# Kernel optimization log

Hardware: AMD Instinct MI355X
Metric: run time of the kernel (lower is better)

Reference implementation:

```python
import jax
import jax.numpy as jnp
import numpy as np

B, N, C_IN, C_OUT, K = 16, 4096, 64, 128, 16
RATIO = 0.25
M = int(RATIO * N)  # 1024 sampled points per cloud
EPS = 1e-5


def setup_inputs() -> dict:
    key = jax.random.key(0)
    ks = jax.random.split(key, 4)
    features = jax.random.normal(ks[0], (B, N, C_IN), dtype=jnp.float32)
    positions = jax.random.normal(ks[1], (B, N, 3), dtype=jnp.float32)
    batch = jnp.repeat(jnp.arange(B, dtype=jnp.int64), N)  # [B*N]
    W = jax.random.normal(ks[2], (C_IN, C_OUT), dtype=jnp.float32) * 0.1
    b = jax.random.normal(ks[3], (C_OUT,), dtype=jnp.float32) * 0.1
    gamma = jnp.ones((C_OUT,), dtype=jnp.float32)
    beta = jnp.zeros((C_OUT,), dtype=jnp.float32)
    return {"features": features, "positions": positions, "batch": batch,
            "W": W, "b": b, "gamma": gamma, "beta": beta}


def _fps_single(pos):
    """Farthest point sampling on one cloud. pos: [N,3] -> indices [M] (start at 0)."""
    def step(carry, _):
        min_d, last = carry
        d = jnp.sum((pos - pos[last]) ** 2, axis=-1)       # [N]
        min_d = jnp.minimum(min_d, d)
        nxt = jnp.argmax(min_d).astype(jnp.int32)
        return (min_d, nxt), nxt
    init = (jnp.full((N,), 1e10, dtype=pos.dtype), jnp.int32(0))
    _, rest = jax.lax.scan(step, init, None, length=M - 1)
    return jnp.concatenate([jnp.zeros((1,), jnp.int32), rest])


def reference(features, positions, batch, W, b, gamma, beta):
    # --- FPS per batch (on positions) ---
    fps_idx = jax.vmap(_fps_single)(positions)                     # [B, M] int32

    # --- MLP: Linear + BatchNorm1d (training-mode batch stats over all B*N points) ---
    h = jnp.einsum('bnc,co->bno', features, W) + b                 # [B, N, C_OUT]
    flat = h.reshape(-1, C_OUT)
    mean = jnp.mean(flat, axis=0)
    var = jnp.mean((flat - mean) ** 2, axis=0)                     # biased, as BN
    hn = (h - mean) * jax.lax.rsqrt(var + EPS) * gamma + beta      # [B, N, C_OUT]

    # --- kNN in FEATURE space: queries = sampled features, keys = all features ---
    q = jnp.take_along_axis(features, fps_idx[..., None], axis=1)  # [B, M, C_IN]
    d2 = (jnp.sum(q * q, -1)[:, :, None]
          + jnp.sum(features * features, -1)[:, None, :]
          - 2.0 * jnp.einsum('bmd,bnd->bmn', q, features))         # [B, M, N]
    _, nbr = jax.lax.top_k(-d2, K)                                 # [B, M, K]

    # --- gather MLP'd features at neighbors, max-pool per sampled point ---
    gathered = jnp.take_along_axis(hn, nbr.reshape(B, M * K)[..., None], axis=1)
    new_features = gathered.reshape(B, M, K, C_OUT).max(axis=2)    # [B, M, C_OUT]

    new_positions = jnp.take_along_axis(positions, fps_idx[..., None], axis=1)  # [B, M, 3]
    new_batch = jnp.take_along_axis(batch.reshape(B, N), fps_idx.astype(jnp.int64), axis=1).reshape(-1)
    return new_features, new_positions, new_batch
```

## Files before the change

kernel.cpp:

```cpp
#include <hip/hip_runtime.h>

#define B_ 16
#define N_ 4096
#define CIN_ 64
#define COUT_ 128
#define K_ 16
#define M_ 1024

typedef float f32x2 __attribute__((ext_vector_type(2)));
typedef unsigned long long u64;

#define DPPF(m, ctrl)                                                          \
  m = fmaxf(m, __int_as_float(__builtin_amdgcn_update_dpp(                     \
                  0, __float_as_int(m), ctrl, 0xF, 0xF, true)))
#define DPPI(e, ctrl)                                                          \
  e = max(e, __builtin_amdgcn_update_dpp(0, e, ctrl, 0xF, 0xF, true))

__device__ __forceinline__ unsigned mono32(float d) {
  unsigned u = __float_as_uint(d);
  return u ^ (unsigned)(((int)u >> 31) | 0x80000000);
}

__device__ __forceinline__ unsigned short f2bf(float x) {
  const unsigned u = __float_as_uint(x);
  return (unsigned short)((u + 0x7FFF + ((u >> 16) & 1)) >> 16);
}
__device__ __forceinline__ float bf2f(unsigned short s) {
  return __uint_as_float((unsigned)s << 16);
}

__global__ __launch_bounds__(512) void mega_kernel(
    const float* __restrict__ pos, const float* __restrict__ features,
    const float* __restrict__ W, const float* __restrict__ bias,
    int* __restrict__ fps_idx, unsigned short* __restrict__ h,
    float* __restrict__ stats, int* __restrict__ prog,
    u64* __restrict__ cand, int S) {
  __shared__ __align__(16) char smem[84 * 1024];
  const int id = blockIdx.x;
  const int t = threadIdx.x;

  if (id < B_) {
    const int b = id;
    float4* P = (float4*)smem;
    volatile u64* red = (volatile u64*)(smem + 65536);
    const float* pb = pos + (size_t)b * N_ * 3;
    if (t < 8) ((u64*)(smem + 65536))[t] = 0;
    for (int i = t; i < N_; i += 512)
      P[i] = make_float4(pb[i * 3], pb[i * 3 + 1], pb[i * 3 + 2], 0.f);
    __syncthreads();
    if (t >= 256) return;
    f32x2 px[8], py[8], pz[8], md[8];
#pragma unroll
    for (int j = 0; j < 8; ++j) {
      const float4 lo = P[t + 512 * j];
      const float4 hi = P[t + 512 * j + 256];
      px[j] = (f32x2){lo.x, hi.x};
      py[j] = (f32x2){lo.y, hi.y};
      pz[j] = (f32x2){lo.z, hi.z};
      md[j] = (f32x2){1e10f, 1e10f};
    }
    if (t == 0) fps_idx[b * M_] = 0;
    const int wv = t >> 6, ln = t & 63;
    const int e0 = 65535 - t;
    float4 lp = P[0];
    for (int step = 1; step < M_; ++step) {
      const f32x2 lx = {lp.x, lp.x}, ly = {lp.y, lp.y}, lz = {lp.z, lp.z};
      float bestd = -1.0f;
      int be = 0;
      {
#pragma clang fp contract(off)
#pragma unroll
        for (int j = 0; j < 8; ++j) {
          const f32x2 dx = px[j] - lx;
          const f32x2 dy = py[j] - ly;
          const f32x2 dz = pz[j] - lz;
          const f32x2 s1 = dx * dx;
          const f32x2 s2 = dy * dy;
          const f32x2 s3 = dz * dz;
          const f32x2 d = (s1 + s2) + s3;
          f32x2 nd;
          nd.x = fminf(md[j].x, d.x);
          nd.y = fminf(md[j].y, d.y);
          md[j] = nd;
          if (nd.x > bestd) { bestd = nd.x; be = e0 - (j << 9); }
          if (nd.y > bestd) { bestd = nd.y; be = e0 - (j << 9) - 256; }
        }
      }
      float m = bestd;
      DPPF(m, 0x111); DPPF(m, 0x112); DPPF(m, 0x114); DPPF(m, 0x118);
      DPPF(m, 0x142); DPPF(m, 0x143);
      const float wm =
          __int_as_float(__builtin_amdgcn_readlane(__float_as_int(m), 63));
      int enc = (bestd == wm) ? be : 0;
      DPPI(enc, 0x111); DPPI(enc, 0x112); DPPI(enc, 0x114); DPPI(enc, 0x118);
      DPPI(enc, 0x142); DPPI(enc, 0x143);
      const int wenc = __builtin_amdgcn_readlane(enc, 63);
      const unsigned tag = (unsigned)(step & 1023);
      volatile u64* rb = red + (step & 1) * 4;
      if (ln == 0)
        rb[wv] = ((u64)__float_as_uint(wm) << 32) | ((u64)tag << 16) |
                 (unsigned)wenc;
      u64 r0, r1, r2, r3;
      for (;;) {
        r0 = rb[0]; r1 = rb[1]; r2 = rb[2]; r3 = rb[3];
        const u64 x = ((r0 >> 16) ^ tag) | ((r1 >> 16) ^ tag) |
                      ((r2 >> 16) ^ tag) | ((r3 >> 16) ^ tag);
        if (!(x & 0x3FF)) break;
      }
      u64 rr = r0 > r1 ? r0 : r1;
      const u64 rc = r2 > r3 ? r2 : r3;
      if (rc > rr) rr = rc;
      const int last = 65535 - (int)(unsigned)(rr & 0xFFFFu);
      lp = P[last];
      if (t == 0) {
        fps_idx[b * M_ + step] = last;
        if ((step & 63) == 63)
          __hip_atomic_store(&prog[b], (step >> 6) + 1, __ATOMIC_RELEASE,
                             __HIP_MEMORY_SCOPE_AGENT);
      }
    }
    return;
  }

  if (id < B_ + 512) {
    const int lid = id - B_;
    float* ls = (float*)smem;
    for (int i = t; i < 256; i += 512) ls[i] = 0.f;
    __syncthreads();
    const int o4 = (t & 31) << 2;
    const int rl = t >> 5;
    const float4 bv = *(const float4*)(bias + o4);
    float4 s4 = {0, 0, 0, 0}, ss4 = {0, 0, 0, 0};
    for (int i = 0; i < 8; ++i) {
      const int r = lid * 128 + rl * 8 + i;
      const float4* fr = (const float4*)(features + (size_t)r * CIN_);
      float4 acc = bv;
#pragma unroll
      for (int c4 = 0; c4 < 16; ++c4) {
        const float4 fv = fr[c4];
        const float* wr = W + (size_t)(c4 * 4) * COUT_ + o4;
        const float4 w0 = *(const float4*)(wr);
        const float4 w1 = *(const float4*)(wr + COUT_);
        const float4 w2 = *(const float4*)(wr + 2 * COUT_);
        const float4 w3 = *(const float4*)(wr + 3 * COUT_);
        acc.x = fmaf(fv.x, w0.x, acc.x); acc.y = fmaf(fv.x, w0.y, acc.y);
        acc.z = fmaf(fv.x, w0.z, acc.z); acc.w = fmaf(fv.x, w0.w, acc.w);
        acc.x = fmaf(fv.y, w1.x, acc.x); acc.y = fmaf(fv.y, w1.y, acc.y);
        acc.z = fmaf(fv.y, w1.z, acc.z); acc.w = fmaf(fv.y, w1.w, acc.w);
        acc.x = fmaf(fv.z, w2.x, acc.x); acc.y = fmaf(fv.z, w2.y, acc.y);
        acc.z = fmaf(fv.z, w2.z, acc.z); acc.w = fmaf(fv.z, w2.w, acc.w);
        acc.x = fmaf(fv.w, w3.x, acc.x); acc.y = fmaf(fv.w, w3.y, acc.y);
        acc.z = fmaf(fv.w, w3.z, acc.z); acc.w = fmaf(fv.w, w3.w, acc.w);
      }
      *(ushort4*)(h + (size_t)r * COUT_ + o4) =
          make_ushort4(f2bf(acc.x), f2bf(acc.y), f2bf(acc.z), f2bf(acc.w));
      s4.x += acc.x; s4.y += acc.y; s4.z += acc.z; s4.w += acc.w;
      ss4.x = fmaf(acc.x, acc.x, ss4.x); ss4.y = fmaf(acc.y, acc.y, ss4.y);
      ss4.z = fmaf(acc.z, acc.z, ss4.z); ss4.w = fmaf(acc.w, acc.w, ss4.w);
    }
    atomicAdd(&ls[o4 + 0], s4.x); atomicAdd(&ls[o4 + 1], s4.y);
    atomicAdd(&ls[o4 + 2], s4.z); atomicAdd(&ls[o4 + 3], s4.w);
    atomicAdd(&ls[128 + o4 + 0], ss4.x); atomicAdd(&ls[128 + o4 + 1], ss4.y);
    atomicAdd(&ls[128 + o4 + 2], ss4.z); atomicAdd(&ls[128 + o4 + 3], ss4.w);
    __syncthreads();
    if (t < 128) {
      atomicAdd(&stats[t], ls[t]);
      atomicAdd(&stats[128 + t], ls[128 + t]);
    }
    return;
  }

  {
    const int kid = id - (B_ + 512);
    const int qt = kid / (B_ * S);
    const int rem = kid % (B_ * S);
    const int b = rem / S;
    const int s = rem % S;
    const int KPS = N_ / S;
    const int KT = KPS / 128;
    float* Qs = (float*)smem;
    float* Ks = (float*)(smem + 16384);
    float* sd2 = (float*)(smem + 49152);
    float* qq = (float*)(smem + 82944);
    float* ff = (float*)(smem + 83200);
    int* qid = (int*)(smem + 83712);
    const float* fb = features + (size_t)b * N_ * CIN_;

    if (t == 0) {
      while (__hip_atomic_load(&prog[b], __ATOMIC_ACQUIRE,
                               __HIP_MEMORY_SCOPE_AGENT) < qt + 1)
        __builtin_amdgcn_s_sleep(16);
    }
    __syncthreads();
    if (t < 64) qid[t] = fps_idx[b * M_ + qt * 64 + t];
    __syncthreads();
#pragma unroll
    for (int st = 0; st < 2; ++st) {
      const int iid = t + 512 * st;
      const int row = iid >> 4, c4 = iid & 15;
      const int pc = (c4 + (row >> 2)) & 15;
      const float4 v = *(const float4*)(fb + (size_t)qid[row] * CIN_ + c4 * 4);
      *(float4*)(&Qs[row * 64 + pc * 4]) = v;
    }
    __syncthreads();
    if (t < 64) {
      float sv = 0.f;
#pragma unroll
      for (int c4 = 0; c4 < 16; ++c4) {
        const int pc = (c4 + (t >> 2)) & 15;
        const float4 v = *(const float4*)(&Qs[t * 64 + pc * 4]);
        sv = fmaf(v.x, v.x, sv); sv = fmaf(v.y, v.y, sv);
        sv = fmaf(v.z, v.z, sv); sv = fmaf(v.w, v.w, sv);
      }
      qq[t] = sv;
    }

    u64 lst[16];
#pragma unroll
    for (int p = 0; p < 16; ++p) lst[p] = ~0ull;
    u64 worst = ~0ull;
    int wpos = 0;

    const int q0 = (t >> 5) * 4;
    const int k0 = (t & 31) * 4;
    const int sq = t >> 3;
    const int ssub = t & 7;

    for (int kt = 0; kt < KT; ++kt) {
      const int kb = s * KPS + kt * 128;
#pragma unroll
      for (int st = 0; st < 4; ++st) {
        const int iid = t + 512 * st;
        const int row = iid >> 4, c4 = iid & 15;
        const int pc = (c4 + (row >> 2)) & 15;
        const float4 v =
            *(const float4*)(fb + (size_t)(kb + row) * CIN_ + c4 * 4);
        *(float4*)(&Ks[row * 64 + pc * 4]) = v;
      }
      __syncthreads();
      if (t < 128) {
        float sv = 0.f;
#pragma unroll
        for (int c4 = 0; c4 < 16; ++c4) {
          const int pc = (c4 + (t >> 2)) & 15;
          const float4 v = *(const float4*)(&Ks[t * 64 + pc * 4]);
          sv = fmaf(v.x, v.x, sv); sv = fmaf(v.y, v.y, sv);
          sv = fmaf(v.z, v.z, sv); sv = fmaf(v.w, v.w, sv);
        }
        ff[t] = sv;
      }
      __syncthreads();
      float acc[4][4];
#pragma unroll
      for (int i = 0; i < 4; ++i)
#pragma unroll
        for (int j = 0; j < 4; ++j) acc[i][j] = 0.f;
#pragma unroll
      for (int c4 = 0; c4 < 16; ++c4) {
        float4 qv[4], kv[4];
#pragma unroll
        for (int i = 0; i < 4; ++i) {
          const int row = q0 + i;
          const int pc = (c4 + (row >> 2)) & 15;
          qv[i] = *(const float4*)(&Qs[row * 64 + pc * 4]);
        }
#pragma unroll
        for (int j = 0; j < 4; ++j) {
          const int row = k0 + j;
          const int pc = (c4 + (row >> 2)) & 15;
          kv[j] = *(const float4*)(&Ks[row * 64 + pc * 4]);
        }
#pragma unroll
        for (int i = 0; i < 4; ++i)
#pragma unroll
          for (int j = 0; j < 4; ++j) {
            acc[i][j] = fmaf(qv[i].x, kv[j].x, acc[i][j]);
            acc[i][j] = fmaf(qv[i].y, kv[j].y, acc[i][j]);
            acc[i][j] = fmaf(qv[i].z, kv[j].z, acc[i][j]);
            acc[i][j] = fmaf(qv[i].w, kv[j].w, acc[i][j]);
          }
      }
#pragma unroll
      for (int i = 0; i < 4; ++i) {
        const float qv = qq[q0 + i];
        float4 o;
        o.x = __fsub_rn(__fadd_rn(qv, ff[k0 + 0]), 2.f * acc[i][0]);
        o.y = __fsub_rn(__fadd_rn(qv, ff[k0 + 1]), 2.f * acc[i][1]);
        o.z = __fsub_rn(__fadd_rn(qv, ff[k0 + 2]), 2.f * acc[i][2]);
        o.w = __fsub_rn(__fadd_rn(qv, ff[k0 + 3]), 2.f * acc[i][3]);
        *(float4*)(&sd2[(q0 + i) * 132 + k0]) = o;
      }
      __syncthreads();
#pragma unroll
      for (int g = 0; g < 4; ++g) {
        const float4 v = *(const float4*)(&sd2[sq * 132 + ssub * 16 + g * 4]);
        const float dv[4] = {v.x, v.y, v.z, v.w};
#pragma unroll
        for (int jj = 0; jj < 4; ++jj) {
          const int key = kb + ssub * 16 + g * 4 + jj;
          const u64 pk = ((u64)mono32(dv[jj]) << 32) | (unsigned)key;
          if (pk < worst) {
#pragma unroll
            for (int p = 0; p < 16; ++p)
              if (p == wpos) lst[p] = pk;
            worst = lst[0]; wpos = 0;
#pragma unroll
            for (int p = 1; p < 16; ++p)
              if (lst[p] > worst) { worst = lst[p]; wpos = p; }
          }
        }
      }
      __syncthreads();
    }
    u64* cb = cand + ((size_t)(b * M_ + qt * 64 + sq) * S + s) * 16;
    for (int r = 0; r < K_; ++r) {
      u64 mn = lst[0];
#pragma unroll
      for (int p = 1; p < 16; ++p)
        if (lst[p] < mn) mn = lst[p];
      u64 m2 = mn;
#pragma unroll
      for (int off = 1; off < 8; off <<= 1) {
        const u64 o = __shfl_xor(m2, off, 64);
        if (o < m2) m2 = o;
      }
      if (mn == m2) {
        bool done = false;
#pragma unroll
        for (int p = 0; p < 16; ++p)
          if (!done && lst[p] == m2) { lst[p] = ~0ull; done = true; }
      }
      if (ssub == 0) cb[r] = m2;
    }
  }
}

__global__ void finalize_kernel(float* __restrict__ stats,
                                const float* __restrict__ gamma,
                                const float* __restrict__ beta) {
  const int o = threadIdx.x;
  const float inv = 1.0f / (float)(B_ * N_);
  const float mean = stats[o] * inv;
  const float var = stats[128 + o] * inv - mean * mean;
  const float r = 1.0f / sqrtf(var + 1e-5f);
  const float sc = gamma[o] * r;
  stats[256 + o] = sc;
  stats[384 + o] = beta[o] - mean * sc;
}

__global__ __launch_bounds__(256) void gather_kernel(
    const unsigned short* __restrict__ h, const float* __restrict__ stats,
    const u64* __restrict__ cand, float* __restrict__ out, int S) {
  const int g = blockIdx.x;
  const int t = threadIdx.x;
  const int S16 = S * 16;
  __shared__ u64 cl[2][128];
  __shared__ int nbi[32];
  const int Q0 = g * 2;
  if (t < 2 * S16) {
    const int qi = t / S16, sl = t % S16;
    cl[qi][sl] = cand[(size_t)(Q0 + qi) * S16 + sl];
  }
  __syncthreads();
  if ((t & 127) == 0) {
    const int qi = t >> 7;
    int ptr[8] = {0, 0, 0, 0, 0, 0, 0, 0};
    for (int r = 0; r < K_; ++r) {
      u64 mn = ~0ull;
      int ms = 0;
      for (int s = 0; s < S; ++s) {
        if (ptr[s] < 16) {
          const u64 v = cl[qi][s * 16 + ptr[s]];
          if (v < mn) { mn = v; ms = s; }
        }
      }
      nbi[qi * 16 + r] = (int)(unsigned)(mn & 0xFFFFFFFFu);
      ptr[ms]++;
    }
  }
  __syncthreads();
  const int q2 = t >> 7, o = t & 127;
  const int Q = Q0 + q2, b = Q >> 10;
  const float sc = stats[256 + o];
  const float sh = stats[384 + o];
  float mx = -3.402823466e38f;
#pragma unroll
  for (int k = 0; k < K_; ++k) {
    const int n = nbi[q2 * 16 + k];
    const float v = fmaf(bf2f(h[((size_t)b * N_ + n) * COUT_ + o]), sc, sh);
    mx = fmaxf(mx, v);
  }
  out[(size_t)Q * COUT_ + o] = mx;
}

__global__ __launch_bounds__(256) void tail_kernel(const float* __restrict__ pos,
                                                   const int* __restrict__ fps_idx,
                                                   float* __restrict__ out,
                                                   int batch_as_i64) {
  const int gid = blockIdx.x * 256 + threadIdx.x;
  const int A = B_ * M_ * COUT_;
  const int P = B_ * M_ * 3;
  if (gid < P) {
    const int Q = gid / 3;
    const int c = gid - Q * 3;
    const int b = Q >> 10;
    const int idx = fps_idx[Q];
    out[A + gid] = pos[((size_t)b * N_ + idx) * 3 + c];
  } else {
    const int Q = gid - P;
    if (Q < B_ * M_) {
      const int b = Q >> 10;
      float* base = out + A + P;
      if (batch_as_i64)
        ((long long*)base)[Q] = (long long)b;
      else
        base[Q] = (float)b;
    }
  }
}

extern "C" void kernel_launch(void* const* d_in, const int* in_sizes, int n_in,
                              void* d_out, int out_size, void* d_ws, size_t ws_size,
                              hipStream_t stream) {
  const float* features = (const float*)d_in[0];
  const float* positions = (const float*)d_in[1];
  const float* W = (const float*)d_in[3];
  const float* bias = (const float*)d_in[4];
  const float* gamma = (const float*)d_in[5];
  const float* beta = (const float*)d_in[6];
  float* out = (float*)d_out;
  unsigned char* ws = (unsigned char*)d_ws;

  int* fps_idx = (int*)ws;
  unsigned short* h = (unsigned short*)(ws + 65536);
  const size_t hoff = 65536 + (size_t)B_ * N_ * COUT_ * 2;
  float* stats = (float*)(ws + hoff);
  int* prog = (int*)(ws + hoff + 2048);
  u64* cand = (u64*)(ws + hoff + 2048 + 256);
  const size_t base = hoff + 2048 + 256;

  int S = 8;
  while (S > 1 && base + (size_t)B_ * M_ * S * 16 * 8 > ws_size) S >>= 1;

  const int rem = out_size - (B_ * M_ * COUT_) - (B_ * M_ * 3);
  const int batch_as_i64 = (rem >= 2 * B_ * M_) ? 1 : 0;

  hipMemsetAsync(stats, 0, 2048 + 256, stream);
  mega_kernel<<<B_ + 512 + 256 * S, 512, 0, stream>>>(
      positions, features, W, bias, fps_idx, h, stats, prog, cand, S);
  finalize_kernel<<<1, 128, 0, stream>>>(stats, gamma, beta);
  gather_kernel<<<B_ * M_ / 2, 256, 0, stream>>>(h, stats, cand, out, S);
  tail_kernel<<<256, 256, 0, stream>>>(positions, fps_idx, out, batch_as_i64);
}
```

Baseline: 1.043 ms.

## Fuse BN finalize, neighbor gather and tail into persistent mega kernel

Moves the BatchNorm finalize step into the last linear block, which it detects with an atomic counter, and signals completion through a flag. The kNN block that finishes last for each query tile now does the candidate merge, the vectorized bf16 gather with max-pool, and the position and batch output writes. This removes three separate kernel launches and their serialization tail. The FPS cross-wave reduction also changes from a spin-poll on tagged LDS slots to __syncthreads, so the idle upper waves now have to loop through matching barriers. This adds inter-block dependencies and the risk of a spin-wait on stats_flag.

New measurement: 1.062 ms. No clear change (+1.8%).

```diff
diff --git a/kernel.cpp b/kernel.cpp
--- a/kernel.cpp
+++ b/kernel.cpp
@@ -20,104 +20,103 @@
   unsigned u = __float_as_uint(d);
   return u ^ (unsigned)(((int)u >> 31) | 0x80000000);
 }
-
 __device__ __forceinline__ unsigned short f2bf(float x) {
   const unsigned u = __float_as_uint(x);
   return (unsigned short)((u + 0x7FFF + ((u >> 16) & 1)) >> 16);
 }
-__device__ __forceinline__ float bf2f(unsigned short s) {
-  return __uint_as_float((unsigned)s << 16);
-}
 
 __global__ __launch_bounds__(512) void mega_kernel(
     const float* __restrict__ pos, const float* __restrict__ features,
     const float* __restrict__ W, const float* __restrict__ bias,
+    const float* __restrict__ gamma, const float* __restrict__ beta,
     int* __restrict__ fps_idx, unsigned short* __restrict__ h,
-    float* __restrict__ stats, int* __restrict__ prog,
-    u64* __restrict__ cand, int S) {
+    float* __restrict__ ctrl, u64* __restrict__ cand,
+    float* __restrict__ out, int S, int batch_as_i64) {
   __shared__ __align__(16) char smem[84 * 1024];
   const int id = blockIdx.x;
   const int t = threadIdx.x;
+  float* stats = ctrl;
+  int* prog = (int*)(ctrl + 512);
+  int* lin_done = (int*)(ctrl + 528);
+  int* stats_flag = (int*)(ctrl + 529);
+  int* qt_done = (int*)(ctrl + 544);
+  const int A = B_ * M_ * COUT_;
+  const int P = B_ * M_ * 3;
 
   if (id < B_) {
     const int b = id;
-    float4* P = (float4*)smem;
-    volatile u64* red = (volatile u64*)(smem + 65536);
+    float4* Pp = (float4*)smem;
+    u64* red = (u64*)(smem + 65536);
     const float* pb = pos + (size_t)b * N_ * 3;
-    if (t < 8) ((u64*)(smem + 65536))[t] = 0;
     for (int i = t; i < N_; i += 512)
-      P[i] = make_float4(pb[i * 3], pb[i * 3 + 1], pb[i * 3 + 2], 0.f);
-    __syncthreads();
-    if (t >= 256) return;
-    f32x2 px[8], py[8], pz[8], md[8];
-#pragma unroll
-    for (int j = 0; j < 8; ++j) {
-      const float4 lo = P[t + 512 * j];
-      const float4 hi = P[t + 512 * j + 256];
-      px[j] = (f32x2){lo.x, hi.x};
-      py[j] = (f32x2){lo.y, hi.y};
-      pz[j] = (f32x2){lo.z, hi.z};
-      md[j] = (f32x2){1e10f, 1e10f};
-    }
-    if (t == 0) fps_idx[b * M_] = 0;
-    const int wv = t >> 6, ln = t & 63;
-    const int e0 = 65535 - t;
-    float4 lp = P[0];
-    for (int step = 1; step < M_; ++step) {
-      const f32x2 lx = {lp.x, lp.x}, ly = {lp.y, lp.y}, lz = {lp.z, lp.z};
-      float bestd = -1.0f;
-      int be = 0;
-      {
+      Pp[i] = make_float4(pb[i * 3], pb[i * 3 + 1], pb[i * 3 + 2], 0.f);
+    __syncthreads();
+    if (t < 256) {
+      f32x2 px[8], py[8], pz[8], md[8];
+#pragma unroll
+      for (int j = 0; j < 8; ++j) {
+        const float4 lo = Pp[t + 512 * j];
+        const float4 hi = Pp[t + 512 * j + 256];
+        px[j] = (f32x2){lo.x, hi.x};
+        py[j] = (f32x2){lo.y, hi.y};
+        pz[j] = (f32x2){lo.z, hi.z};
+        md[j] = (f32x2){1e10f, 1e10f};
+      }
+      if (t == 0) fps_idx[b * M_] = 0;
+      const int wv = t >> 6, ln = t & 63;
+      const int e0 = 65535 - t;
+      float4 lp = Pp[0];
+      for (int step = 1; step < M_; ++step) {
+        const f32x2 lx = {lp.x, lp.x}, ly = {lp.y, lp.y}, lz = {lp.z, lp.z};
+        float bestd = -1.0f;
+        int be = 0;
+        {
 #pragma clang fp contract(off)
 #pragma unroll
-        for (int j = 0; j < 8; ++j) {
-          const f32x2 dx = px[j] - lx;
-          const f32x2 dy = py[j] - ly;
-          const f32x2 dz = pz[j] - lz;
-          const f32x2 s1 = dx * dx;
-          const f32x2 s2 = dy * dy;
-          const f32x2 s3 = dz * dz;
-          const f32x2 d = (s1 + s2) + s3;
-          f32x2 nd;
-          nd.x = fminf(md[j].x, d.x);
-          nd.y = fminf(md[j].y, d.y);
-          md[j] = nd;
-          if (nd.x > bestd) { bestd = nd.x; be = e0 - (j << 9); }
-          if (nd.y > bestd) { bestd = nd.y; be = e0 - (j << 9) - 256; }
-        }
-      }
-      float m = bestd;
-      DPPF(m, 0x111); DPPF(m, 0x112); DPPF(m, 0x114); DPPF(m, 0x118);
-      DPPF(m, 0x142); DPPF(m, 0x143);
-      const float wm =
-          __int_as_float(__builtin_amdgcn_readlane(__float_as_int(m), 63));
-      int enc = (bestd == wm) ? be : 0;
-      DPPI(enc, 0x111); DPPI(enc, 0x112); DPPI(enc, 0x114); DPPI(enc, 0x118);
-      DPPI(enc, 0x142); DPPI(enc, 0x143);
-      const int wenc = __builtin_amdgcn_readlane(enc, 63);
-      const unsigned tag = (unsigned)(step & 1023);
-      volatile u64* rb = red + (step & 1) * 4;
-      if (ln == 0)
-        rb[wv] = ((u64)__float_as_uint(wm) << 32) | ((u64)tag << 16) |
-                 (unsigned)wenc;
-      u64 r0, r1, r2, r3;
-      for (;;) {
-        r0 = rb[0]; r1 = rb[1]; r2 = rb[2]; r3 = rb[3];
-        const u64 x = ((r0 >> 16) ^ tag) | ((r1 >> 16) ^ tag) |
-                      ((r2 >> 16) ^ tag) | ((r3 >> 16) ^ tag);
-        if (!(x & 0x3FF)) break;
-      }
-      u64 rr = r0 > r1 ? r0 : r1;
-      const u64 rc = r2 > r3 ? r2 : r3;
-      if (rc > rr) rr = rc;
-      const int last = 65535 - (int)(unsigned)(rr & 0xFFFFu);
-      lp = P[last];
-      if (t == 0) {
-        fps_idx[b * M_ + step] = last;
-        if ((step & 63) == 63)
-          __hip_atomic_store(&prog[b], (step >> 6) + 1, __ATOMIC_RELEASE,
-                             __HIP_MEMORY_SCOPE_AGENT);
-      }
+          for (int j = 0; j < 8; ++j) {
+            const f32x2 dx = px[j] - lx;
+            const f32x2 dy = py[j] - ly;
+            const f32x2 dz = pz[j] - lz;
+            const f32x2 s1 = dx * dx;
+            const f32x2 s2 = dy * dy;
+            const f32x2 s3 = dz * dz;
+            const f32x2 d = (s1 + s2) + s3;
+            f32x2 nd;
+            nd.x = fminf(md[j].x, d.x);
+            nd.y = fminf(md[j].y, d.y);
+            md[j] = nd;
+            if (nd.x > bestd) { bestd = nd.x; be = e0 - (j << 9); }
+            if (nd.y > bestd) { bestd = nd.y; be = e0 - (j << 9) - 256; }
+          }
+        }
+        float m = bestd;
+        DPPF(m, 0x111); DPPF(m, 0x112); DPPF(m, 0x114); DPPF(m, 0x118);
+        DPPF(m, 0x142); DPPF(m, 0x143);
+        const float wm =
+            __int_as_float(__builtin_amdgcn_readlane(__float_as_int(m), 63));
+        int enc = (bestd == wm) ? be : 0;
+        DPPI(enc, 0x111); DPPI(enc, 0x112); DPPI(enc, 0x114); DPPI(enc, 0x118);
+        DPPI(enc, 0x142); DPPI(enc, 0x143);
+        const int wenc = __builtin_amdgcn_readlane(enc, 63);
+        if (ln == 0)
+          red[(step & 1) * 4 + wv] =
+              ((u64)__float_as_uint(wm) << 32) | (unsigned)wenc;
+        __syncthreads();
+        const u64* rb = &red[(step & 1) * 4];
+        u64 rr = rb[0] > rb[1] ? rb[0] : rb[1];
+        const u64 r2 = rb[2] > rb[3] ? rb[2] : rb[3];
+        if (r2 > rr) rr = r2;
+        const int last = 65535 - (int)(unsigned)(rr & 0xFFFFu);
+        lp = Pp[last];
+        if (t == 0) {
+          fps_idx[b * M_ + step] = last;
+          if ((step & 63) == 63)
+            __hip_atomic_store(&prog[b], (step >> 6) + 1, __ATOMIC_RELEASE,
+                               __HIP_MEMORY_SCOPE_AGENT);
+        }
+      }
+    } else {
+      for (int step = 1; step < M_; ++step) __syncthreads();
     }
     return;
   }
@@ -167,6 +166,26 @@
       atomicAdd(&stats[t], ls[t]);
       atomicAdd(&stats[128 + t], ls[128 + t]);
     }
+    __syncthreads();
+    int* lastf = (int*)(smem + 1024);
+    if (t == 0)
+      *lastf = (__hip_atomic_fetch_add(lin_done, 1, __ATOMIC_ACQ_REL,
+                                       __HIP_MEMORY_SCOPE_AGENT) == 511);
+    __syncthreads();
+    if (!*lastf) return;
+    if (t < 128) {
+      const float inv = 1.0f / (float)(B_ * N_);
+      const float mean = stats[t] * inv;
+      const float var = stats[128 + t] * inv - mean * mean;
+      const float r = 1.0f / sqrtf(var + 1e-5f);
+      const float sc = gamma[t] * r;
+      stats[256 + t] = sc;
+      stats[384 + t] = beta[t] - mean * sc;
+    }
+    __syncthreads();
+    if (t == 0)
+      __hip_atomic_store(stats_flag, 1, __ATOMIC_RELEASE,
+                         __HIP_MEMORY_SCOPE_AGENT);
     return;
   }
 
@@ -184,6 +203,7 @@
     float* qq = (float*)(smem + 82944);
     float* ff = (float*)(smem + 83200);
     int* qid = (int*)(smem + 83712);
+    int* mflag = (int*)(smem + 83968);
     const float* fb = features + (size_t)b * N_ * CIN_;
 
     if (t == 0) {
@@ -332,84 +352,84 @@
       }
       if (ssub == 0) cb[r] = m2;
     }
-  }
-}
-
-__global__ void finalize_kernel(float* __restrict__ stats,
-                                const float* __restrict__ gamma,
-                                const float* __restrict__ beta) {
-  const int o = threadIdx.x;
-  const float inv = 1.0f / (float)(B_ * N_);
-  const float mean = stats[o] * inv;
-  const float var = stats[128 + o] * inv - mean * mean;
-  const float r = 1.0f / sqrtf(var + 1e-5f);
-  const float sc = gamma[o] * r;
-  stats[256 + o] = sc;
-  stats[384 + o] = beta[o] - mean * sc;
-}
-
-__global__ __launch_bounds__(256) void gather_kernel(
-    const unsigned short* __restrict__ h, const float* __restrict__ stats,
-    const u64* __restrict__ cand, float* __restrict__ out, int S) {
-  const int g = blockIdx.x;
-  const int t = threadIdx.x;
-  const int S16 = S * 16;
-  __shared__ u64 cl[2][128];
-  __shared__ int nbi[32];
-  const int Q0 = g * 2;
-  if (t < 2 * S16) {
-    const int qi = t / S16, sl = t % S16;
-    cl[qi][sl] = cand[(size_t)(Q0 + qi) * S16 + sl];
-  }
-  __syncthreads();
-  if ((t & 127) == 0) {
-    const int qi = t >> 7;
-    int ptr[8] = {0, 0, 0, 0, 0, 0, 0, 0};
-    for (int r = 0; r < K_; ++r) {
-      u64 mn = ~0ull;
-      int ms = 0;
-      for (int s = 0; s < S; ++s) {
-        if (ptr[s] < 16) {
-          const u64 v = cl[qi][s * 16 + ptr[s]];
-          if (v < mn) { mn = v; ms = s; }
-        }
-      }
-      nbi[qi * 16 + r] = (int)(unsigned)(mn & 0xFFFFFFFFu);
-      ptr[ms]++;
-    }
-  }
-  __syncthreads();
-  const int q2 = t >> 7, o = t & 127;
-  const int Q = Q0 + q2, b = Q >> 10;
-  const float sc = stats[256 + o];
-  const float sh = stats[384 + o];
-  float mx = -3.402823466e38f;
-#pragma unroll
-  for (int k = 0; k < K_; ++k) {
-    const int n = nbi[q2 * 16 + k];
-    const float v = fmaf(bf2f(h[((size_t)b * N_ + n) * COUT_ + o]), sc, sh);
-    mx = fmaxf(mx, v);
-  }
-  out[(size_t)Q * COUT_ + o] = mx;
-}
-
-__global__ __launch_bounds__(256) void tail_kernel(const float* __restrict__ pos,
-                                                   const int* __restrict__ fps_idx,
-                                                   float* __restrict__ out,
-                                                   int batch_as_i64) {
-  const int gid = blockIdx.x * 256 + threadIdx.x;
-  const int A = B_ * M_ * COUT_;
-  const int P = B_ * M_ * 3;
-  if (gid < P) {
-    const int Q = gid / 3;
-    const int c = gid - Q * 3;
-    const int b = Q >> 10;
-    const int idx = fps_idx[Q];
-    out[A + gid] = pos[((size_t)b * N_ + idx) * 3 + c];
-  } else {
-    const int Q = gid - P;
-    if (Q < B_ * M_) {
-      const int b = Q >> 10;
+    __syncthreads();
+    if (t == 0)
+      *mflag = (__hip_atomic_fetch_add(&qt_done[b * 16 + qt], 1,
+                                       __ATOMIC_ACQ_REL,
+                                       __HIP_MEMORY_SCOPE_AGENT) == S - 1);
+    __syncthreads();
+    if (!*mflag) return;
+
+    u64* cl = (u64*)smem;
+    int* nbi = (int*)(smem + 65536);
+    float* scsh = (float*)(smem + 69632);
+    if (t == 0) {
+      while (__hip_atomic_load(stats_flag, __ATOMIC_ACQUIRE,
+                               __HIP_MEMORY_SCOPE_AGENT) == 0)
+        __builtin_amdgcn_s_sleep(8);
+    }
+    __syncthreads();
+    const int S16 = S * 16;
+    const u64* cg = cand + (size_t)(b * M_ + qt * 64) * S16;
+    for (int i = t; i < 64 * S16; i += 512) cl[i] = cg[i];
+    if (t < 256) scsh[t] = stats[256 + t];
+    __syncthreads();
+    if (t < 64) {
+      int ptr[8] = {0, 0, 0, 0, 0, 0, 0, 0};
+      for (int r = 0; r < K_; ++r) {
+        u64 mn = ~0ull;
+        int ms = 0;
+        for (int ss = 0; ss < S; ++ss) {
+          if (ptr[ss] < 16) {
+            const u64 v = cl[t * S16 + ss * 16 + ptr[ss]];
+            if (v < mn) { mn = v; ms = ss; }
+          }
+        }
+        nbi[t * 16 + r] = (int)(unsigned)(mn & 0xFFFFFFFFu);
+        ptr[ms]++;
+      }
+    }
+    __syncthreads();
+    {
+      const int q = t >> 3;
+      const int c0 = (t & 7) * 16;
+      float sc[16], sh[16], mx[16];
+#pragma unroll
+      for (int i = 0; i < 16; ++i) {
+        sc[i] = scsh[c0 + i];
+        sh[i] = scsh[128 + c0 + i];
+        mx[i] = -3.402823466e38f;
+      }
+#pragma unroll
+      for (int k = 0; k < K_; ++k) {
+        const int n = nbi[q * 16 + k];
+        const uint4* hr =
+            (const uint4*)(h + ((size_t)b * N_ + n) * COUT_ + c0);
+        const uint4 h0 = hr[0];
+        const uint4 h1 = hr[1];
+        const unsigned hu[8] = {h0.x, h0.y, h0.z, h0.w, h1.x, h1.y, h1.z, h1.w};
+#pragma unroll
+        for (int i = 0; i < 8; ++i) {
+          const float lo = __uint_as_float(hu[i] << 16);
+          const float hi = __uint_as_float(hu[i] & 0xFFFF0000u);
+          mx[2 * i] = fmaxf(mx[2 * i], fmaf(lo, sc[2 * i], sh[2 * i]));
+          mx[2 * i + 1] = fmaxf(mx[2 * i + 1], fmaf(hi, sc[2 * i + 1], sh[2 * i + 1]));
+        }
+      }
+      float* ob = out + (size_t)(b * M_ + qt * 64 + q) * COUT_ + c0;
+#pragma unroll
+      for (int i = 0; i < 4; ++i)
+        *(float4*)(ob + 4 * i) =
+            make_float4(mx[4 * i], mx[4 * i + 1], mx[4 * i + 2], mx[4 * i + 3]);
+    }
+    if (t < 64) {
+      const int q = t;
+      const int Q = b * M_ + qt * 64 + q;
+      const int idx = qid[q];
+      const float* pr = pos + ((size_t)b * N_ + idx) * 3;
+      out[A + Q * 3 + 0] = pr[0];
+      out[A + Q * 3 + 1] = pr[1];
+      out[A + Q * 3 + 2] = pr[2];
       float* base = out + A + P;
       if (batch_as_i64)
         ((long long*)base)[Q] = (long long)b;
@@ -434,10 +454,9 @@
   int* fps_idx = (int*)ws;
   unsigned short* h = (unsigned short*)(ws + 65536);
   const size_t hoff = 65536 + (size_t)B_ * N_ * COUT_ * 2;
-  float* stats = (float*)(ws + hoff);
-  int* prog = (int*)(ws + hoff + 2048);
-  u64* cand = (u64*)(ws + hoff + 2048 + 256);
-  const size_t base = hoff + 2048 + 256;
+  float* ctrl = (float*)(ws + hoff);
+  u64* cand = (u64*)(ws + hoff + 4096);
+  const size_t base = hoff + 4096;
 
   int S = 8;
   while (S > 1 && base + (size_t)B_ * M_ * S * 16 * 8 > ws_size) S >>= 1;
@@ -445,10 +464,8 @@
   const int rem = out_size - (B_ * M_ * COUT_) - (B_ * M_ * 3);
   const int batch_as_i64 = (rem >= 2 * B_ * M_) ? 1 : 0;
 
-  hipMemsetAsync(stats, 0, 2048 + 256, stream);
+  hipMemsetAsync(ctrl, 0, 4096, stream);
   mega_kernel<<<B_ + 512 + 256 * S, 512, 0, stream>>>(
-      positions, features, W, bias, fps_idx, h, stats, prog, cand, S);
-  finalize_kernel<<<1, 128, 0, stream>>>(stats, gamma, beta);
-  gather_kernel<<<B_ * M_ / 2, 256, 0, stream>>>(h, stats, cand, out, S);
-  tail_kernel<<<256, 256, 0, stream>>>(positions, fps_idx, out, batch_as_i64);
+      positions, features, W, bias, gamma, beta, fps_idx, h, ctrl, cand, out,
+      S, batch_as_i64);
 }
```

## Broadcast winner coordinates through reduction slots and fuse finalize/gather/tail kernels

Applied to the files above, without the earlier changes.

In the FPS loop, the lane holding each wave's winning point now selects that point's coordinates from its own registers and publishes them to LDS next to the max/index. This removes the dependent LDS lookup of the selected point after the cross-wave reduction on every step, and the full position copy into LDS is dropped. Separately, the BN finalize, neighbor gather and tail copy kernels are merged into one launch, each block recomputing scale and shift, which cuts two kernel launches. The cost is more LDS writes and polling reads per FPS step plus extra select instructions, and the validity check now depends on a second tag word per slot.

After: 1.690 ms. 62.0% more time.

```diff
diff --git a/kernel.cpp b/kernel.cpp
--- a/kernel.cpp
+++ b/kernel.cpp
@@ -20,60 +20,54 @@
   unsigned u = __float_as_uint(d);
   return u ^ (unsigned)(((int)u >> 31) | 0x80000000);
 }
-
 __device__ __forceinline__ unsigned short f2bf(float x) {
   const unsigned u = __float_as_uint(x);
   return (unsigned short)((u + 0x7FFF + ((u >> 16) & 1)) >> 16);
 }
-__device__ __forceinline__ float bf2f(unsigned short s) {
-  return __uint_as_float((unsigned)s << 16);
-}
 
 __global__ __launch_bounds__(512) void mega_kernel(
     const float* __restrict__ pos, const float* __restrict__ features,
     const float* __restrict__ W, const float* __restrict__ bias,
     int* __restrict__ fps_idx, unsigned short* __restrict__ h,
-    float* __restrict__ stats, int* __restrict__ prog,
-    u64* __restrict__ cand, int S) {
+    float* __restrict__ ctrl, u64* __restrict__ cand, int S) {
   __shared__ __align__(16) char smem[84 * 1024];
   const int id = blockIdx.x;
   const int t = threadIdx.x;
+  float* stats = ctrl;
+  int* prog = (int*)(ctrl + 512);
 
   if (id < B_) {
     const int b = id;
-    float4* P = (float4*)smem;
-    volatile u64* red = (volatile u64*)(smem + 65536);
+    volatile u64* slots = (volatile u64*)smem;
     const float* pb = pos + (size_t)b * N_ * 3;
-    if (t < 8) ((u64*)(smem + 65536))[t] = 0;
-    for (int i = t; i < N_; i += 512)
-      P[i] = make_float4(pb[i * 3], pb[i * 3 + 1], pb[i * 3 + 2], 0.f);
+    if (t < 32) ((u64*)smem)[t] = 0;
     __syncthreads();
     if (t >= 256) return;
     f32x2 px[8], py[8], pz[8], md[8];
 #pragma unroll
     for (int j = 0; j < 8; ++j) {
-      const float4 lo = P[t + 512 * j];
-      const float4 hi = P[t + 512 * j + 256];
-      px[j] = (f32x2){lo.x, hi.x};
-      py[j] = (f32x2){lo.y, hi.y};
-      pz[j] = (f32x2){lo.z, hi.z};
+      const float* r0 = pb + (size_t)(t + 512 * j) * 3;
+      const float* r1 = pb + (size_t)(t + 512 * j + 256) * 3;
+      px[j] = (f32x2){r0[0], r1[0]};
+      py[j] = (f32x2){r0[1], r1[1]};
+      pz[j] = (f32x2){r0[2], r1[2]};
       md[j] = (f32x2){1e10f, 1e10f};
     }
     if (t == 0) fps_idx[b * M_] = 0;
     const int wv = t >> 6, ln = t & 63;
     const int e0 = 65535 - t;
-    float4 lp = P[0];
+    float lx = pb[0], ly = pb[1], lz = pb[2];
     for (int step = 1; step < M_; ++step) {
-      const f32x2 lx = {lp.x, lp.x}, ly = {lp.y, lp.y}, lz = {lp.z, lp.z};
+      const f32x2 vlx = {lx, lx}, vly = {ly, ly}, vlz = {lz, lz};
       float bestd = -1.0f;
       int be = 0;
       {
 #pragma clang fp contract(off)
 #pragma unroll
         for (int j = 0; j < 8; ++j) {
-          const f32x2 dx = px[j] - lx;
-          const f32x2 dy = py[j] - ly;
-          const f32x2 dz = pz[j] - lz;
+          const f32x2 dx = px[j] - vlx;
+          const f32x2 dy = py[j] - vly;
+          const f32x2 dz = pz[j] - vlz;
           const f32x2 s1 = dx * dx;
           const f32x2 s2 = dy * dy;
           const f32x2 s3 = dz * dz;
@@ -86,6 +80,26 @@
           if (nd.y > bestd) { bestd = nd.y; be = e0 - (j << 9) - 256; }
         }
       }
+      const unsigned u = (unsigned)(65535 - be - t) >> 8;
+      const int b0 = u & 2, b1 = u & 4, b2 = u & 8, hh = u & 1;
+      f32x2 xs, ys, zs;
+      {
+        const f32x2 x01 = b0 ? px[1] : px[0], x23 = b0 ? px[3] : px[2];
+        const f32x2 x45 = b0 ? px[5] : px[4], x67 = b0 ? px[7] : px[6];
+        const f32x2 x03 = b1 ? x23 : x01, x47 = b1 ? x67 : x45;
+        xs = b2 ? x47 : x03;
+        const f32x2 y01 = b0 ? py[1] : py[0], y23 = b0 ? py[3] : py[2];
+        const f32x2 y45 = b0 ? py[5] : py[4], y67 = b0 ? py[7] : py[6];
+        const f32x2 y03 = b1 ? y23 : y01, y47 = b1 ? y67 : y45;
+        ys = b2 ? y47 : y03;
+        const f32x2 z01 = b0 ? pz[1] : pz[0], z23 = b0 ? pz[3] : pz[2];
+        const f32x2 z45 = b0 ? pz[5] : pz[4], z67 = b0 ? pz[7] : pz[6];
+        const f32x2 z03 = b1 ? z23 : z01, z47 = b1 ? z67 : z45;
+        zs = b2 ? z47 : z03;
+      }
+      const float wx = hh ? xs.y : xs.x;
+      const float wy = hh ? ys.y : ys.x;
+      const float wz = hh ? zs.y : zs.x;
       float m = bestd;
       DPPF(m, 0x111); DPPF(m, 0x112); DPPF(m, 0x114); DPPF(m, 0x118);
       DPPF(m, 0x142); DPPF(m, 0x143);
@@ -96,24 +110,40 @@
       DPPI(enc, 0x142); DPPI(enc, 0x143);
       const int wenc = __builtin_amdgcn_readlane(enc, 63);
       const unsigned tag = (unsigned)(step & 1023);
-      volatile u64* rb = red + (step & 1) * 4;
+      volatile u64* sb = slots + (step & 1) * 16 + wv * 4;
       if (ln == 0)
-        rb[wv] = ((u64)__float_as_uint(wm) << 32) | ((u64)tag << 16) |
-                 (unsigned)wenc;
-      u64 r0, r1, r2, r3;
+        sb[0] = ((u64)__float_as_uint(wm) << 32) | ((u64)tag << 16) |
+                (unsigned)wenc;
+      if (be == wenc) {
+        sb[1] = ((u64)__float_as_uint(wy) << 32) | __float_as_uint(wx);
+        sb[2] = ((u64)tag << 32) | __float_as_uint(wz);
+      }
+      volatile u64* base = slots + (step & 1) * 16;
+      u64 T[4], XY[4], ZC[4];
       for (;;) {
-        r0 = rb[0]; r1 = rb[1]; r2 = rb[2]; r3 = rb[3];
-        const u64 x = ((r0 >> 16) ^ tag) | ((r1 >> 16) ^ tag) |
-                      ((r2 >> 16) ^ tag) | ((r3 >> 16) ^ tag);
-        if (!(x & 0x3FF)) break;
-      }
-      u64 rr = r0 > r1 ? r0 : r1;
-      const u64 rc = r2 > r3 ? r2 : r3;
-      if (rc > rr) rr = rc;
-      const int last = 65535 - (int)(unsigned)(rr & 0xFFFFu);
-      lp = P[last];
+        unsigned bad = 0;
+#pragma unroll
+        for (int w = 0; w < 4; ++w) {
+          T[w] = base[w * 4 + 0];
+          XY[w] = base[w * 4 + 1];
+          ZC[w] = base[w * 4 + 2];
+          bad |= (((unsigned)(T[w] >> 16)) & 1023u) ^ tag;
+          bad |= ((unsigned)(ZC[w] >> 32)) ^ tag;
+        }
+        if (!bad) break;
+      }
+      const bool c01 = T[0] > T[1], c23 = T[2] > T[3];
+      const u64 ta = c01 ? T[0] : T[1], xa = c01 ? XY[0] : XY[1],
+                za = c01 ? ZC[0] : ZC[1];
+      const u64 tb = c23 ? T[2] : T[3], xb = c23 ? XY[2] : XY[3],
+                zb = c23 ? ZC[2] : ZC[3];
+      const bool cab = ta > tb;
+      const u64 rr = cab ? ta : tb, rxy = cab ? xa : xb, rzc = cab ? za : zb;
+      lx = __uint_as_float((unsigned)rxy);
+      ly = __uint_as_float((unsigned)(rxy >> 32));
+      lz = __uint_as_float((unsigned)rzc);
       if (t == 0) {
-        fps_idx[b * M_ + step] = last;
+        fps_idx[b * M_ + step] = 65535 - (int)(unsigned)(rr & 0xFFFFu);
         if ((step & 63) == 63)
           __hip_atomic_store(&prog[b], (step >> 6) + 1, __ATOMIC_RELEASE,
                              __HIP_MEMORY_SCOPE_AGENT);
@@ -335,27 +365,53 @@
   }
 }
 
-__global__ void finalize_kernel(float* __restrict__ stats,
-                                const float* __restrict__ gamma,
-                                const float* __restrict__ beta) {
-  const int o = threadIdx.x;
-  const float inv = 1.0f / (float)(B_ * N_);
-  const float mean = stats[o] * inv;
-  const float var = stats[128 + o] * inv - mean * mean;
-  const float r = 1.0f / sqrtf(var + 1e-5f);
-  const float sc = gamma[o] * r;
-  stats[256 + o] = sc;
-  stats[384 + o] = beta[o] - mean * sc;
-}
-
-__global__ __launch_bounds__(256) void gather_kernel(
-    const unsigned short* __restrict__ h, const float* __restrict__ stats,
-    const u64* __restrict__ cand, float* __restrict__ out, int S) {
+__global__ __launch_bounds__(256) void gather_tail_kernel(
+    const float* __restrict__ pos, const int* __restrict__ fps_idx,
+    const unsigned short* __restrict__ h, const float* __restrict__ ctrl,
+    const float* __restrict__ gamma, const float* __restrict__ beta,
+    const u64* __restrict__ cand, float* __restrict__ out, int S,
+    int batch_as_i64) {
   const int g = blockIdx.x;
   const int t = threadIdx.x;
-  const int S16 = S * 16;
+  const int A = B_ * M_ * COUT_;
+  const int P = B_ * M_ * 3;
+  if (g >= B_ * M_ / 2) {
+    const int gid2 = (g - B_ * M_ / 2) * 256 + t;
+    for (int i = 0; i < 16; ++i) {
+      const int gid = gid2 + 4096 * i;
+      if (gid < P) {
+        const int Q = gid / 3;
+        const int c = gid - Q * 3;
+        const int b = Q >> 10;
+        const int idx = fps_idx[Q];
+        out[A + gid] = pos[((size_t)b * N_ + idx) * 3 + c];
+      } else {
+        const int Q = gid - P;
+        if (Q < B_ * M_) {
+          const int b = Q >> 10;
+          float* base = out + A + P;
+          if (batch_as_i64)
+            ((long long*)base)[Q] = (long long)b;
+          else
+            base[Q] = (float)b;
+        }
+      }
+    }
+    return;
+  }
   __shared__ u64 cl[2][128];
   __shared__ int nbi[32];
+  __shared__ float scsh[256];
+  if (t < 128) {
+    const float inv = 1.0f / (float)(B_ * N_);
+    const float mean = ctrl[t] * inv;
+    const float var = ctrl[128 + t] * inv - mean * mean;
+    const float r = 1.0f / sqrtf(var + 1e-5f);
+    const float sc = gamma[t] * r;
+    scsh[t] = sc;
+    scsh[128 + t] = beta[t] - mean * sc;
+  }
+  const int S16 = S * 16;
   const int Q0 = g * 2;
   if (t < 2 * S16) {
     const int qi = t / S16, sl = t % S16;
@@ -381,42 +437,18 @@
   __syncthreads();
   const int q2 = t >> 7, o = t & 127;
   const int Q = Q0 + q2, b = Q >> 10;
-  const float sc = stats[256 + o];
-  const float sh = stats[384 + o];
+  const float sc = scsh[o];
+  const float sh = scsh[128 + o];
   float mx = -3.402823466e38f;
 #pragma unroll
   for (int k = 0; k < K_; ++k) {
     const int n = nbi[q2 * 16 + k];
-    const float v = fmaf(bf2f(h[((size_t)b * N_ + n) * COUT_ + o]), sc, sh);
+    const float v = fmaf(
+        __uint_as_float((unsigned)h[((size_t)b * N_ + n) * COUT_ + o] << 16),
+        sc, sh);
     mx = fmaxf(mx, v);
   }
   out[(size_t)Q * COUT_ + o] = mx;
-}
-
-__global__ __launch_bounds__(256) void tail_kernel(const float* __restrict__ pos,
-                                                   const int* __restrict__ fps_idx,
-                                                   float* __restrict__ out,
-                                                   int batch_as_i64) {
-  const int gid = blockIdx.x * 256 + threadIdx.x;
-  const int A = B_ * M_ * COUT_;
-  const int P = B_ * M_ * 3;
-  if (gid < P) {
-    const int Q = gid / 3;
-    const int c = gid - Q * 3;
-    const int b = Q >> 10;
-    const int idx = fps_idx[Q];
-    out[A + gid] = pos[((size_t)b * N_ + idx) * 3 + c];
-  } else {
-    const int Q = gid - P;
-    if (Q < B_ * M_) {
-      const int b = Q >> 10;
-      float* base = out + A + P;
-      if (batch_as_i64)
-        ((long long*)base)[Q] = (long long)b;
-      else
-        base[Q] = (float)b;
-    }
-  }
 }
 
 extern "C" void kernel_launch(void* const* d_in, const int* in_sizes, int n_in,
@@ -434,10 +466,9 @@
   int* fps_idx = (int*)ws;
   unsigned short* h = (unsigned short*)(ws + 65536);
   const size_t hoff = 65536 + (size_t)B_ * N_ * COUT_ * 2;
-  float* stats = (float*)(ws + hoff);
-  int* prog = (int*)(ws + hoff + 2048);
-  u64* cand = (u64*)(ws + hoff + 2048 + 256);
-  const size_t base = hoff + 2048 + 256;
+  float* ctrl = (float*)(ws + hoff);
+  u64* cand = (u64*)(ws + hoff + 4096);
+  const size_t base = hoff + 4096;
 
   int S = 8;
   while (S > 1 && base + (size_t)B_ * M_ * S * 16 * 8 > ws_size) S >>= 1;
@@ -445,10 +476,9 @@
   const int rem = out_size - (B_ * M_ * COUT_) - (B_ * M_ * 3);
   const int batch_as_i64 = (rem >= 2 * B_ * M_) ? 1 : 0;
 
-  hipMemsetAsync(stats, 0, 2048 + 256, stream);
+  hipMemsetAsync(ctrl, 0, 4096, stream);
   mega_kernel<<<B_ + 512 + 256 * S, 512, 0, stream>>>(
-      positions, features, W, bias, fps_idx, h, stats, prog, cand, S);
-  finalize_kernel<<<1, 128, 0, stream>>>(stats, gamma, beta);
-  gather_kernel<<<B_ * M_ / 2, 256, 0, stream>>>(h, stats, cand, out, S);
-  tail_kernel<<<256, 256, 0, stream>>>(positions, fps_idx, out, batch_as_i64);
+      positions, features, W, bias, fps_idx, h, ctrl, cand, S);
+  gather_tail_kernel<<<B_ * M_ / 2 + 16, 256, 0, stream>>>(
+      positions, fps_idx, h, ctrl, gamma, beta, cand, out, S, batch_as_i64);
 }
```
